# Kernel optimization log

Measured on AMD Instinct MI355X. Metric: run time of the kernel, lower is better.

## Reference

```python
import jax, jax.numpy as jnp
import numpy as np

HEADS = 8
DIM_HEAD = 64
DIM = 512
MAX_POS_EMB = 512
SCALE = DIM_HEAD ** -0.5


def setup_inputs() -> dict:
    key = jax.random.key(0)
    ks = jax.random.split(key, 6)
    B, N = 2, 2048
    inner = HEADS * DIM_HEAD  # 512
    x = jax.random.normal(ks[0], (B, N, DIM), dtype=jnp.float32)
    # torch Linear weights stored as [out, in]; we keep [in, out] for x @ W
    Wq = jax.random.normal(ks[1], (DIM, inner), dtype=jnp.float32) * (DIM ** -0.5)
    Wkv = jax.random.normal(ks[2], (DIM, 2 * inner), dtype=jnp.float32) * (DIM ** -0.5)
    Wo = jax.random.normal(ks[3], (inner, DIM), dtype=jnp.float32) * (inner ** -0.5)
    bo = jax.random.normal(ks[4], (DIM,), dtype=jnp.float32) * 0.02
    rel_emb = jax.random.normal(ks[5], (2 * MAX_POS_EMB + 1, DIM_HEAD), dtype=jnp.float32)
    return {"x": x, "Wq": Wq, "Wkv": Wkv, "Wo": Wo, "bo": bo, "rel_emb": rel_emb}


def reference(x, Wq, Wkv, Wo, bo, rel_emb):
    B, N, _ = x.shape
    h, d = HEADS, DIM_HEAD
    q = x @ Wq                                # [B, N, h*d]
    kv = x @ Wkv                              # [B, N, 2*h*d]
    k, v = jnp.split(kv, 2, axis=-1)
    to_heads = lambda t: t.reshape(B, N, h, d).transpose(0, 2, 1, 3)  # [B, h, N, d]
    q, k, v = to_heads(q), to_heads(k), to_heads(v)

    dots = jnp.einsum('bhid,bhjd->bhij', q, k) * SCALE  # [B, h, N, N]

    # relative positional bias: dist clamped to [-max, max], shifted to [0, 2*max]
    seq = jnp.arange(N)
    dist = jnp.clip(seq[:, None] - seq[None, :], -MAX_POS_EMB, MAX_POS_EMB) + MAX_POS_EMB
    rel = rel_emb[dist]                                 # [N, N, d]
    pos_attn = jnp.einsum('bhnd,njd->bhnj', q, rel) * SCALE
    dots = dots + pos_attn

    attn = jax.nn.softmax(dots, axis=-1)
    out = jnp.einsum('bhij,bhjd->bhid', attn, v)        # [B, h, N, d]
    out = out.transpose(0, 2, 1, 3).reshape(B, N, h * d)
    return out @ Wo + bo
```

## Files before the change

kernel.cpp:

```cpp
#include <hip/hip_runtime.h>
#include <hip/hip_bf16.h>
#include <stdint.h>

#define HEADS 8
#define DHEAD 64
#define DIM 512
#define NSEQ 2048
#define BATCH 2
#define NROWS (BATCH * NSEQ)
#define QKV_N 1536
#define REL_ROWS 1025
#define REL_PITCH 1088
#define NSPLIT 2
#define KV_PER_SPLIT (NSEQ / NSPLIT)

static constexpr float SCALE_LOG2E = 0.125f * 1.4426950408889634f;

typedef __attribute__((ext_vector_type(8))) short bf16x8;
typedef __attribute__((ext_vector_type(4))) float f32x4;

__device__ __forceinline__ uint16_t f2bf(float f) {
    union { float f; uint32_t u; } v{f};
    uint32_t r = (v.u + 0x7FFFu + ((v.u >> 16) & 1u)) >> 16;
    return (uint16_t)r;
}
__device__ __forceinline__ float bf2f(uint16_t u) {
    union { uint32_t u; float f; } v{(uint32_t)u << 16};
    return v.f;
}

__global__ void prep_misc(const float* __restrict__ x, const float* __restrict__ rel,
                          uint16_t* __restrict__ xb, uint16_t* __restrict__ relb) {
    int total = NROWS * DIM + REL_PITCH * DHEAD;
    for (int idx = blockIdx.x * blockDim.x + threadIdx.x; idx < total; idx += gridDim.x * blockDim.x) {
        if (idx < NROWS * DIM) {
            xb[idx] = f2bf(x[idx]);
        } else {
            int i2 = idx - NROWS * DIM;
            relb[i2] = (i2 < REL_ROWS * DHEAD) ? f2bf(rel[i2]) : (uint16_t)0;
        }
    }
}

__global__ void prep_w(const float* __restrict__ Wq, const float* __restrict__ Wkv,
                       const float* __restrict__ Wo,
                       uint16_t* __restrict__ Wqkv_t, uint16_t* __restrict__ Wo_t) {
    __shared__ float tile[32][33];
    int bid = blockIdx.x;
    const float* src; uint16_t* dst; int J, ti, tj;
    if (bid < 256)      { src = Wq;  dst = Wqkv_t;             J = 512;  ti = bid >> 4;        tj = bid & 15; }
    else if (bid < 768) { int b = bid - 256; src = Wkv; dst = Wqkv_t + 512 * 512; J = 1024; ti = b >> 5; tj = b & 31; }
    else                { int b = bid - 768; src = Wo;  dst = Wo_t;   J = 512;  ti = b >> 4;        tj = b & 15; }
    int tx = threadIdx.x & 31, ty = threadIdx.x >> 5;
    int k0 = ti * 32, j0 = tj * 32;
    #pragma unroll
    for (int i = 0; i < 4; i++) tile[ty + 8 * i][tx] = src[(size_t)(k0 + ty + 8 * i) * J + j0 + tx];
    __syncthreads();
    #pragma unroll
    for (int i = 0; i < 4; i++) dst[(size_t)(j0 + ty + 8 * i) * 512 + k0 + tx] = f2bf(tile[tx][ty + 8 * i]);
}

template <bool BF16_OUT>
__global__ __launch_bounds__(256) void gemm128(const uint16_t* __restrict__ A,
                                               const uint16_t* __restrict__ Bt,
                                               void* __restrict__ Cout,
                                               const float* __restrict__ bias,
                                               int K, int ldc) {
    __shared__ char lds[32768];
    char* ldsA = lds;
    char* ldsB = lds + 16384;
    int m0 = blockIdx.x * 128, n0 = blockIdx.y * 128;
    int t = threadIdx.x, lane = t & 63, w = t >> 6;
    int wr = w >> 1, wc = w & 1;
    int l15 = lane & 15, lh = lane >> 4;
    f32x4 acc[4][4] = {};
    for (int k0 = 0; k0 < K; k0 += 64) {
        __syncthreads();
        {
            int row = t >> 3, ch = t & 7;
            #pragma unroll
            for (int p = 0; p < 4; p++) {
                int r = row + 32 * p;
                bf16x8 va = *(const bf16x8*)(A + (size_t)(m0 + r) * K + k0 + ch * 8);
                *(bf16x8*)(ldsA + r * 128 + ((ch * 16) ^ ((r & 7) << 4))) = va;
                bf16x8 vb = *(const bf16x8*)(Bt + (size_t)(n0 + r) * K + k0 + ch * 8);
                *(bf16x8*)(ldsB + r * 128 + ((ch * 16) ^ ((r & 7) << 4))) = vb;
            }
        }
        __syncthreads();
        #pragma unroll
        for (int kk = 0; kk < 2; kk++) {
            bf16x8 a[4], b[4];
            #pragma unroll
            for (int mi = 0; mi < 4; mi++) {
                int m = wr * 64 + mi * 16 + l15;
                a[mi] = *(const bf16x8*)(ldsA + m * 128 + ((kk * 64 + lh * 16) ^ ((m & 7) << 4)));
            }
            #pragma unroll
            for (int ni = 0; ni < 4; ni++) {
                int n = wc * 64 + ni * 16 + l15;
                b[ni] = *(const bf16x8*)(ldsB + n * 128 + ((kk * 64 + lh * 16) ^ ((n & 7) << 4)));
            }
            #pragma unroll
            for (int mi = 0; mi < 4; mi++)
                #pragma unroll
                for (int ni = 0; ni < 4; ni++)
                    acc[mi][ni] = __builtin_amdgcn_mfma_f32_16x16x32_bf16(a[mi], b[ni], acc[mi][ni], 0, 0, 0);
        }
    }
    #pragma unroll
    for (int mi = 0; mi < 4; mi++)
        #pragma unroll
        for (int ni = 0; ni < 4; ni++)
            #pragma unroll
            for (int i = 0; i < 4; i++) {
                int m = m0 + wr * 64 + mi * 16 + lh * 4 + i;
                int n = n0 + wc * 64 + ni * 16 + l15;
                float v = acc[mi][ni][i];
                if constexpr (BF16_OUT) ((uint16_t*)Cout)[(size_t)m * ldc + n] = f2bf(v);
                else                    ((float*)Cout)[(size_t)m * ldc + n] = v + bias[n];
            }
}

__global__ __launch_bounds__(256) void qrel_gemm(const uint16_t* __restrict__ QKV,
                                                 const uint16_t* __restrict__ relb,
                                                 uint16_t* __restrict__ qrel) {
    __shared__ char lds[16384];
    char* ldsA = lds;
    char* ldsB = lds + 8192;
    int h = blockIdx.y;
    int r0 = blockIdx.x * 64;
    int t = threadIdx.x, lane = t & 63, w = t >> 6;
    int l15 = lane & 15, lh = lane >> 4;
    {
        int row = t >> 3, ch = t & 7;
        #pragma unroll
        for (int p = 0; p < 2; p++) {
            int r = row + 32 * p;
            bf16x8 v = *(const bf16x8*)(QKV + (size_t)(r0 + r) * QKV_N + h * 64 + ch * 8);
            *(bf16x8*)(ldsA + r * 128 + ((ch * 16) ^ ((r & 7) << 4))) = v;
        }
    }
    __syncthreads();
    bf16x8 afrag[2];
    #pragma unroll
    for (int kk = 0; kk < 2; kk++) {
        int m = w * 16 + l15;
        afrag[kk] = *(const bf16x8*)(ldsA + m * 128 + ((kk * 64 + lh * 16) ^ ((m & 7) << 4)));
    }
    for (int pb = 0; pb < REL_PITCH / 64; pb++) {
        int p0 = pb * 64;
        __syncthreads();
        {
            int row = t >> 3, ch = t & 7;
            #pragma unroll
            for (int p = 0; p < 2; p++) {
                int r = row + 32 * p;
                bf16x8 v = *(const bf16x8*)(relb + (size_t)(p0 + r) * 64 + ch * 8);
                *(bf16x8*)(ldsB + r * 128 + ((ch * 16) ^ ((r & 7) << 4))) = v;
            }
        }
        __syncthreads();
        f32x4 acc[4] = {};
        #pragma unroll
        for (int kk = 0; kk < 2; kk++)
            #pragma unroll
            for (int ni = 0; ni < 4; ni++) {
                int n = ni * 16 + l15;
                bf16x8 b = *(const bf16x8*)(ldsB + n * 128 + ((kk * 64 + lh * 16) ^ ((n & 7) << 4)));
                acc[ni] = __builtin_amdgcn_mfma_f32_16x16x32_bf16(afrag[kk], b, acc[ni], 0, 0, 0);
            }
        #pragma unroll
        for (int ni = 0; ni < 4; ni++)
            #pragma unroll
            for (int i = 0; i < 4; i++) {
                int rr = r0 + w * 16 + lh * 4 + i;
                int p = p0 + ni * 16 + l15;
                qrel[((size_t)h * NROWS + rr) * REL_PITCH + p] = f2bf(acc[ni][i]);
            }
    }
}

__global__ __launch_bounds__(512, 4) void attn_kernel(const uint16_t* __restrict__ QKV,
                                                      const uint16_t* __restrict__ qrel,
                                                      float* __restrict__ Opart,
                                                      float* __restrict__ mlpart) {
    __shared__ char lds[53248];
    char* ldsQ = lds;
    char* ldsKV = lds + 16384;

    int flat = blockIdx.x + 16 * (blockIdx.y + 8 * blockIdx.z);
    int x = (flat & 7) * 64 + (flat >> 3);
    int qb = x & 15, h = (x >> 4) & 7, z = x >> 7;
    int b = z >> 1, sp = z & 1;

    int t = threadIdx.x, lane = t & 63, w = t >> 6;
    int l15 = lane & 15, lh = lane >> 4;
    int row = t >> 3, ch = t & 7;
    int n0 = qb * 128;
    int kvbase = sp * KV_PER_SPLIT;
    size_t rowQ = (size_t)b * NSEQ + n0;

    {
        int buf = t >> 8, idx = t & 255;
        uint32_t val = (idx < 16) ? 0x3F803F80u : 0u;
        char* p = ldsKV + buf * 18432 + 8192 + 8192 + (idx >> 4) * 128 + (idx & 15) * 8;
        *(uint32_t*)(p) = val;
        *(uint32_t*)(p + 4) = val;
    }

    #pragma unroll
    for (int p = 0; p < 2; p++) {
        int r = row + 64 * p;
        bf16x8 v = *(const bf16x8*)(QKV + (rowQ + r) * QKV_N + h * 64 + ch * 8);
        *(bf16x8*)(ldsQ + r * 128 + ((ch * 16) ^ ((r & 7) << 4))) = v;
    }
    __syncthreads();
    bf16x8 qf[2];
    #pragma unroll
    for (int kk = 0; kk < 2; kk++) {
        int m = w * 16 + l15;
        qf[kk] = *(const bf16x8*)(ldsQ + m * 128 + ((kk * 64 + lh * 16) ^ ((m & 7) << 4)));
    }
    char* myP = ldsQ + w * 2048;

    f32x4 oacc[5] = {};
    float mrow[4];
    #pragma unroll
    for (int i = 0; i < 4; i++) mrow[i] = -INFINITY;

    const uint16_t* qbase = qrel + ((size_t)h * NROWS + (size_t)b * NSEQ) * REL_PITCH;
    uint32_t rowbase[4];
    #pragma unroll
    for (int i = 0; i < 4; i++) rowbase[i] = (uint32_t)(n0 + w * 16 + lh * 4 + i) * REL_PITCH + 512;

    auto load_kv = [&](int tile, bf16x8& kr, bf16x8& vr) {
        size_t gro = ((size_t)b * NSEQ + kvbase + tile * 64 + row) * QKV_N + h * 64 + ch * 8;
        kr = *(const bf16x8*)(QKV + gro + 512);
        vr = *(const bf16x8*)(QKV + gro + 1024);
    };
    auto scatter_kv = [&](int tile, bf16x8& kr, bf16x8& vr) {
        char* ldsK = ldsKV + (tile & 1) * 18432;
        char* ldsV = ldsK + 8192;
        *(bf16x8*)(ldsK + row * 128 + ((ch * 16) ^ ((row & 7) << 4))) = kr;
        #pragma unroll
        for (int dd = 0; dd < 8; dd++) {
            int d = ch * 8 + dd;
            int s = dd ^ ch;
            *(uint16_t*)(ldsV + d * 128 + 2 * (row ^ (s << 3))) = (uint16_t)vr[dd];
        }
    };
    auto load_g = [&](int tile, uint16_t* g) {
        int kv0 = kvbase + tile * 64;
        int rel0 = n0 - kv0;
        if (rel0 <= -640) {
            #pragma unroll
            for (int i = 0; i < 4; i++) {
                uint16_t v = qbase[rowbase[i] - 512];
                #pragma unroll
                for (int nf = 0; nf < 4; nf++) g[nf * 4 + i] = v;
            }
        } else if (rel0 >= 576) {
            #pragma unroll
            for (int i = 0; i < 4; i++) {
                uint16_t v = qbase[rowbase[i] + 512];
                #pragma unroll
                for (int nf = 0; nf < 4; nf++) g[nf * 4 + i] = v;
            }
        } else {
            #pragma unroll
            for (int i = 0; i < 4; i++) {
                int nmk = (n0 + w * 16 + lh * 4 + i) - kv0;
                #pragma unroll
                for (int nf = 0; nf < 4; nf++) {
                    int d = nmk - (nf * 16 + l15);
                    d = d < -512 ? -512 : (d > 512 ? 512 : d);
                    g[nf * 4 + i] = qbase[rowbase[i] + d];
                }
            }
        }
    };

    const int NT = KV_PER_SPLIT / 64;
    uint16_t gA[16], gB[16];
    bf16x8 krA, vrA, krB, vrB;

    load_kv(0, krA, vrA);
    load_g(0, gA);
    scatter_kv(0, krA, vrA);
    load_kv(1, krB, vrB);
    load_g(1, gB);

    auto body = [&](int tt, bf16x8& kS, bf16x8& vS, uint16_t* gS, bf16x8& kO, bf16x8& vO) {
        char* ldsK = ldsKV + (tt & 1) * 18432;
        char* ldsV = ldsK + 8192;
        __syncthreads();
        if (tt + 2 < NT) load_kv(tt + 2, kS, vS);

        f32x4 sacc[4] = {};
        __builtin_amdgcn_s_setprio(1);
        #pragma unroll
        for (int kk = 0; kk < 2; kk++)
            #pragma unroll
            for (int nf = 0; nf < 4; nf++) {
                int n = nf * 16 + l15;
                bf16x8 kfv = *(const bf16x8*)(ldsK + n * 128 + ((kk * 64 + lh * 16) ^ ((n & 7) << 4)));
                sacc[nf] = __builtin_amdgcn_mfma_f32_16x16x32_bf16(qf[kk], kfv, sacc[nf], 0, 0, 0);
            }
        __builtin_amdgcn_s_setprio(0);

        #pragma unroll
        for (int nf = 0; nf < 4; nf++)
            #pragma unroll
            for (int i = 0; i < 4; i++)
                sacc[nf][i] += bf2f(gS[nf * 4 + i]);
        if (tt + 2 < NT) load_g(tt + 2, gS);

        float lmax = sacc[0][0];
        #pragma unroll
        for (int nf = 0; nf < 4; nf++)
            #pragma unroll
            for (int i = 0; i < 4; i++) lmax = fmaxf(lmax, sacc[nf][i]);
        float mmin = fminf(fminf(mrow[0], mrow[1]), fminf(mrow[2], mrow[3]));
        if (!__all(lmax <= mmin + 64.0f)) {
            #pragma unroll
            for (int i = 0; i < 4; i++) {
                float mx = fmaxf(fmaxf(sacc[0][i], sacc[1][i]), fmaxf(sacc[2][i], sacc[3][i]));
                mx = fmaxf(mx, __shfl_xor(mx, 1));
                mx = fmaxf(mx, __shfl_xor(mx, 2));
                mx = fmaxf(mx, __shfl_xor(mx, 4));
                mx = fmaxf(mx, __shfl_xor(mx, 8));
                float mnew = fmaxf(mrow[i], mx);
                float alpha = exp2f((mrow[i] - mnew) * SCALE_LOG2E);
                mrow[i] = mnew;
                #pragma unroll
                for (int nf = 0; nf < 5; nf++) oacc[nf][i] *= alpha;
            }
        }

        #pragma unroll
        for (int i = 0; i < 4; i++) {
            int r = lh * 4 + i;
            int rsw = (r & 7) << 4;
            #pragma unroll
            for (int nf = 0; nf < 4; nf++) {
                float p = exp2f((sacc[nf][i] - mrow[i]) * SCALE_LOG2E);
                uint32_t pb;
                asm("v_cvt_pk_bf16_f32 %0, %1, %2" : "=v"(pb) : "v"(p), "v"(p));
                *(uint16_t*)(myP + r * 128 + (((nf * 16 + l15) * 2) ^ rsw)) = (uint16_t)pb;
            }
        }

        asm volatile("s_waitcnt lgkmcnt(0)" ::: "memory");
        __builtin_amdgcn_sched_barrier(0);
        __builtin_amdgcn_s_setprio(1);
        #pragma unroll
        for (int kk = 0; kk < 2; kk++) {
            bf16x8 pa = *(const bf16x8*)(myP + l15 * 128 + ((kk * 64 + lh * 16) ^ ((l15 & 7) << 4)));
            #pragma unroll
            for (int nf = 0; nf < 5; nf++) {
                int d = nf * 16 + l15;
                int sd = (d & 7) ^ ((d >> 3) & 7);
                bf16x8 vb = *(const bf16x8*)(ldsV + d * 128 + 16 * ((kk * 4 + lh) ^ sd));
                oacc[nf] = __builtin_amdgcn_mfma_f32_16x16x32_bf16(pa, vb, oacc[nf], 0, 0, 0);
            }
        }
        __builtin_amdgcn_s_setprio(0);

        if (tt + 1 < NT) scatter_kv(tt + 1, kO, vO);
    };

    #pragma unroll 1
    for (int tt2 = 0; tt2 < NT; tt2 += 2) {
        body(tt2,     krA, vrA, gA, krB, vrB);
        body(tt2 + 1, krB, vrB, gB, krA, vrA);
    }

    size_t rbase = ((size_t)(sp * BATCH + b) * HEADS + h) * NSEQ;
    #pragma unroll
    for (int nf = 0; nf < 4; nf++)
        #pragma unroll
        for (int i = 0; i < 4; i++) {
            int r = n0 + w * 16 + lh * 4 + i;
            Opart[(rbase + r) * 64 + nf * 16 + l15] = oacc[nf][i];
        }
    if (l15 == 0) {
        #pragma unroll
        for (int i = 0; i < 4; i++) {
            int r = n0 + w * 16 + lh * 4 + i;
            mlpart[(rbase + r) * 2]     = mrow[i];
            mlpart[(rbase + r) * 2 + 1] = oacc[4][i];
        }
    }
}

__global__ __launch_bounds__(256) void combine_kernel(const float* __restrict__ Opart,
                                                      const float* __restrict__ mlpart,
                                                      uint16_t* __restrict__ attO) {
    int lane = threadIdx.x & 63;
    int R = blockIdx.x * 4 + (threadIdx.x >> 6);
    const int SPSTRIDE = BATCH * HEADS * NSEQ;
    float m1 = mlpart[(size_t)R * 2], l1 = mlpart[(size_t)R * 2 + 1];
    float m2 = mlpart[((size_t)SPSTRIDE + R) * 2], l2 = mlpart[((size_t)SPSTRIDE + R) * 2 + 1];
    float M = fmaxf(m1, m2);
    float w1 = exp2f((m1 - M) * SCALE_LOG2E);
    float w2 = exp2f((m2 - M) * SCALE_LOG2E);
    float Linv = 1.f / (l1 * w1 + l2 * w2);
    float o1 = Opart[(size_t)R * 64 + lane];
    float o2 = Opart[((size_t)SPSTRIDE + R) * 64 + lane];
    float o = (o1 * w1 + o2 * w2) * Linv;
    int bh = R >> 11, n = R & 2047;
    int b = bh >> 3, hh = bh & 7;
    attO[((size_t)(b * NSEQ + n)) * DIM + hh * 64 + lane] = f2bf(o);
}

extern "C" void kernel_launch(void* const* d_in, const int* in_sizes, int n_in,
                              void* d_out, int out_size, void* d_ws, size_t ws_size,
                              hipStream_t stream) {
    const float* x   = (const float*)d_in[0];
    const float* Wq  = (const float*)d_in[1];
    const float* Wkv = (const float*)d_in[2];
    const float* Wo  = (const float*)d_in[3];
    const float* bo  = (const float*)d_in[4];
    const float* rel = (const float*)d_in[5];
    char* ws = (char*)d_ws;
    uint16_t* Xb     = (uint16_t*)(ws);
    float*    mlp    = (float*)(ws);
    uint16_t* Wqkv_t = (uint16_t*)(ws + 4194304);
    uint16_t* Wo_t   = (uint16_t*)(ws + 5767168);
    uint16_t* relb   = (uint16_t*)(ws + 6291456);
    uint16_t* QKV    = (uint16_t*)(ws + 6430720);
    uint16_t* attO   = (uint16_t*)(ws + 19013632);
    uint16_t* qrel   = (uint16_t*)(ws + 23207936);
    float*    Opart  = (float*)(ws + 94511104);

    prep_misc<<<2048, 256, 0, stream>>>(x, rel, Xb, relb);
    prep_w<<<1024, 256, 0, stream>>>(Wq, Wkv, Wo, Wqkv_t, Wo_t);
    gemm128<true><<<dim3(32, 12), 256, 0, stream>>>(Xb, Wqkv_t, QKV, nullptr, 512, QKV_N);
    qrel_gemm<<<dim3(64, 8), 256, 0, stream>>>(QKV, relb, qrel);
    attn_kernel<<<dim3(16, 8, 4), 512, 0, stream>>>(QKV, qrel, Opart, mlp);
    combine_kernel<<<8192, 256, 0, stream>>>(Opart, mlp, attO);
    gemm128<false><<<dim3(32, 4), 256, 0, stream>>>(attO, Wo_t, (float*)d_out, bo, 512, DIM);
}
```

Measured before the change: 159.0 us.

## Stage relative-bias window through LDS with vectorized global loads

Each thread previously gathered 16 scattered bf16 relative-bias values per KV tile straight from global memory. Now each thread loads two contiguous 8-element vectors of the diagonal window of the qrel row into registers, writes them into a new per-wave LDS region, and the MMA lanes read their bias values back from LDS with a reversed index. The aim is to replace many scalar uncoalesced global loads with a few 16-byte loads. In exchange, LDS use per block grows from 53 KB to about 70 KB, which may lower the number of resident blocks, and each tile adds LDS traffic.

Result: slower. 209.0 us (+31.4%).

```diff
diff --git a/kernel.cpp b/kernel.cpp
--- a/kernel.cpp
+++ b/kernel.cpp
@@ -17,6 +17,7 @@
 static constexpr float SCALE_LOG2E = 0.125f * 1.4426950408889634f;
 
 typedef __attribute__((ext_vector_type(8))) short bf16x8;
+typedef __attribute__((ext_vector_type(4))) short bf16x4;
 typedef __attribute__((ext_vector_type(4))) float f32x4;
 
 __device__ __forceinline__ uint16_t f2bf(float f) {
@@ -185,9 +186,10 @@
                                                       const uint16_t* __restrict__ qrel,
                                                       float* __restrict__ Opart,
                                                       float* __restrict__ mlpart) {
-    __shared__ char lds[53248];
+    __shared__ __align__(16) char lds[70656];
     char* ldsQ = lds;
     char* ldsKV = lds + 16384;
+    char* ldsW = lds + 53248;
 
     int flat = blockIdx.x + 16 * (blockIdx.y + 8 * blockIdx.z);
     int x = (flat & 7) * 64 + (flat >> 3);
@@ -197,6 +199,7 @@
     int t = threadIdx.x, lane = t & 63, w = t >> 6;
     int l15 = lane & 15, lh = lane >> 4;
     int row = t >> 3, ch = t & 7;
+    int q4 = t & 3;
     int n0 = qb * 128;
     int kvbase = sp * KV_PER_SPLIT;
     size_t rowQ = (size_t)b * NSEQ + n0;
@@ -223,6 +226,7 @@
         qf[kk] = *(const bf16x8*)(ldsQ + m * 128 + ((kk * 64 + lh * 16) ^ ((m & 7) << 4)));
     }
     char* myP = ldsQ + w * 2048;
+    char* myW = ldsW + w * 2176;
 
     f32x4 oacc[5] = {};
     float mrow[4];
@@ -230,9 +234,8 @@
     for (int i = 0; i < 4; i++) mrow[i] = -INFINITY;
 
     const uint16_t* qbase = qrel + ((size_t)h * NROWS + (size_t)b * NSEQ) * REL_PITCH;
-    uint32_t rowbase[4];
-    #pragma unroll
-    for (int i = 0; i < 4; i++) rowbase[i] = (uint32_t)(n0 + w * 16 + lh * 4 + i) * REL_PITCH + 512;
+    const uint16_t* qrow_n = qbase + (size_t)(n0 + (t >> 2)) * REL_PITCH + 512;
+    int nmk_w = n0 + (t >> 2) - kvbase;
 
     auto load_kv = [&](int tile, bf16x8& kr, bf16x8& vr) {
         size_t gro = ((size_t)b * NSEQ + kvbase + tile * 64 + row) * QKV_N + h * 64 + ch * 8;
@@ -250,52 +253,65 @@
             *(uint16_t*)(ldsV + d * 128 + 2 * (row ^ (s << 3))) = (uint16_t)vr[dd];
         }
     };
-    auto load_g = [&](int tile, uint16_t* g) {
-        int kv0 = kvbase + tile * 64;
-        int rel0 = n0 - kv0;
-        if (rel0 <= -640) {
-            #pragma unroll
-            for (int i = 0; i < 4; i++) {
-                uint16_t v = qbase[rowbase[i] - 512];
+    auto load_w = [&](int tile, bf16x8* wreg) {
+        int dbase = nmk_w - tile * 64 - 63;
+        #pragma unroll
+        for (int p = 0; p < 2; p++) {
+            int dlo = dbase + q4 * 16 + p * 8;
+            if (dlo >= -512 && dlo <= 505) {
+                wreg[p] = *(const bf16x8*)(qrow_n + dlo);
+            } else if (dlo <= -520) {
+                uint16_t v = qrow_n[-512];
                 #pragma unroll
-                for (int nf = 0; nf < 4; nf++) g[nf * 4 + i] = v;
-            }
-        } else if (rel0 >= 576) {
-            #pragma unroll
-            for (int i = 0; i < 4; i++) {
-                uint16_t v = qbase[rowbase[i] + 512];
+                for (int e = 0; e < 8; e++) wreg[p][e] = (short)v;
+            } else if (dlo >= 512) {
+                uint16_t v = qrow_n[512];
                 #pragma unroll
-                for (int nf = 0; nf < 4; nf++) g[nf * 4 + i] = v;
-            }
-        } else {
-            #pragma unroll
-            for (int i = 0; i < 4; i++) {
-                int nmk = (n0 + w * 16 + lh * 4 + i) - kv0;
+                for (int e = 0; e < 8; e++) wreg[p][e] = (short)v;
+            } else {
                 #pragma unroll
-                for (int nf = 0; nf < 4; nf++) {
-                    int d = nmk - (nf * 16 + l15);
+                for (int e = 0; e < 8; e++) {
+                    int d = dlo + e;
                     d = d < -512 ? -512 : (d > 512 ? 512 : d);
-                    g[nf * 4 + i] = qbase[rowbase[i] + d];
+                    wreg[p][e] = (short)qrow_n[d];
                 }
             }
         }
     };
+    auto write_w = [&](bf16x8* wreg) {
+        char* base = ldsW + (t >> 6) * 2176 + ((t >> 2) & 15) * 136 + q4 * 32;
+        const bf16x4* w0 = (const bf16x4*)&wreg[0];
+        const bf16x4* w1 = (const bf16x4*)&wreg[1];
+        *(bf16x4*)(base)      = w0[0];
+        *(bf16x4*)(base + 8)  = w0[1];
+        *(bf16x4*)(base + 16) = w1[0];
+        *(bf16x4*)(base + 24) = w1[1];
+    };
 
     const int NT = KV_PER_SPLIT / 64;
-    uint16_t gA[16], gB[16];
-    bf16x8 krA, vrA, krB, vrB;
+    bf16x8 krA, vrA, krB, vrB, wrA[2], wrB[2];
 
     load_kv(0, krA, vrA);
-    load_g(0, gA);
+    load_w(0, wrA);
     scatter_kv(0, krA, vrA);
+    write_w(wrA);
     load_kv(1, krB, vrB);
-    load_g(1, gB);
-
-    auto body = [&](int tt, bf16x8& kS, bf16x8& vS, uint16_t* gS, bf16x8& kO, bf16x8& vO) {
+    load_w(1, wrB);
+
+    auto body = [&](int tt, bf16x8& kS, bf16x8& vS, bf16x8* wS,
+                    bf16x8& kO, bf16x8& vO, bf16x8* wO) {
         char* ldsK = ldsKV + (tt & 1) * 18432;
         char* ldsV = ldsK + 8192;
         __syncthreads();
-        if (tt + 2 < NT) load_kv(tt + 2, kS, vS);
+        if (tt + 2 < NT) { load_kv(tt + 2, kS, vS); load_w(tt + 2, wS); }
+
+        uint16_t gb[16];
+        #pragma unroll
+        for (int nf = 0; nf < 4; nf++)
+            #pragma unroll
+            for (int i = 0; i < 4; i++)
+                gb[nf * 4 + i] = *(const uint16_t*)(myW + (lh * 4 + i) * 136
+                                                    + (63 - nf * 16 - l15) * 2);
 
         f32x4 sacc[4] = {};
         __builtin_amdgcn_s_setprio(1);
@@ -313,8 +329,7 @@
         for (int nf = 0; nf < 4; nf++)
             #pragma unroll
             for (int i = 0; i < 4; i++)
-                sacc[nf][i] += bf2f(gS[nf * 4 + i]);
-        if (tt + 2 < NT) load_g(tt + 2, gS);
+                sacc[nf][i] += bf2f(gb[nf * 4 + i]);
 
         float lmax = sacc[0][0];
         #pragma unroll
@@ -367,13 +382,13 @@
         }
         __builtin_amdgcn_s_setprio(0);
 
-        if (tt + 1 < NT) scatter_kv(tt + 1, kO, vO);
+        if (tt + 1 < NT) { scatter_kv(tt + 1, kO, vO); write_w(wO); }
     };
 
     #pragma unroll 1
     for (int tt2 = 0; tt2 < NT; tt2 += 2) {
-        body(tt2,     krA, vrA, gA, krB, vrB);
-        body(tt2 + 1, krB, vrB, gB, krA, vrA);
+        body(tt2,     krA, vrA, wrA, krB, vrB, wrB);
+        body(tt2 + 1, krB, vrB, wrB, krA, vrA, wrA);
     }
 
     size_t rbase = ((size_t)(sp * BATCH + b) * HEADS + h) * NSEQ;
```

## Fuse relative-position bias into attention kernel via on-the-fly MFMA and lane permute

Applied to the files above, without the earlier changes.

Removes the separate qrel_gemm kernel, which wrote a large per-head q·rel table (roughly 71 MB bf16) and had attention gather from it. Each attention tile now computes q·rel for the 80 relative offsets it needs using extra MFMAs on rel embedding rows loaded from global memory. A ds_bpermute then realigns the diagonal (Toeplitz) structure into the score layout. This trades a large memory write and gather for extra MFMA work, cross-lane shuffles and uncached rel loads inside the attention loop. It also simplifies the KV pipeline from a two-tile software prefetch to a single-tile one.

New measurement: 167.5 us. +5.4%, slower.

```diff
diff --git a/kernel.cpp b/kernel.cpp
--- a/kernel.cpp
+++ b/kernel.cpp
@@ -10,7 +10,7 @@
 #define NROWS (BATCH * NSEQ)
 #define QKV_N 1536
 #define REL_ROWS 1025
-#define REL_PITCH 1088
+#define REL_PITCH_ROWS 1088
 #define NSPLIT 2
 #define KV_PER_SPLIT (NSEQ / NSPLIT)
 
@@ -24,14 +24,10 @@
     uint32_t r = (v.u + 0x7FFFu + ((v.u >> 16) & 1u)) >> 16;
     return (uint16_t)r;
 }
-__device__ __forceinline__ float bf2f(uint16_t u) {
-    union { uint32_t u; float f; } v{(uint32_t)u << 16};
-    return v.f;
-}
 
 __global__ void prep_misc(const float* __restrict__ x, const float* __restrict__ rel,
                           uint16_t* __restrict__ xb, uint16_t* __restrict__ relb) {
-    int total = NROWS * DIM + REL_PITCH * DHEAD;
+    int total = NROWS * DIM + REL_PITCH_ROWS * DHEAD;
     for (int idx = blockIdx.x * blockDim.x + threadIdx.x; idx < total; idx += gridDim.x * blockDim.x) {
         if (idx < NROWS * DIM) {
             xb[idx] = f2bf(x[idx]);
@@ -122,67 +118,8 @@
             }
 }
 
-__global__ __launch_bounds__(256) void qrel_gemm(const uint16_t* __restrict__ QKV,
-                                                 const uint16_t* __restrict__ relb,
-                                                 uint16_t* __restrict__ qrel) {
-    __shared__ char lds[16384];
-    char* ldsA = lds;
-    char* ldsB = lds + 8192;
-    int h = blockIdx.y;
-    int r0 = blockIdx.x * 64;
-    int t = threadIdx.x, lane = t & 63, w = t >> 6;
-    int l15 = lane & 15, lh = lane >> 4;
-    {
-        int row = t >> 3, ch = t & 7;
-        #pragma unroll
-        for (int p = 0; p < 2; p++) {
-            int r = row + 32 * p;
-            bf16x8 v = *(const bf16x8*)(QKV + (size_t)(r0 + r) * QKV_N + h * 64 + ch * 8);
-            *(bf16x8*)(ldsA + r * 128 + ((ch * 16) ^ ((r & 7) << 4))) = v;
-        }
-    }
-    __syncthreads();
-    bf16x8 afrag[2];
-    #pragma unroll
-    for (int kk = 0; kk < 2; kk++) {
-        int m = w * 16 + l15;
-        afrag[kk] = *(const bf16x8*)(ldsA + m * 128 + ((kk * 64 + lh * 16) ^ ((m & 7) << 4)));
-    }
-    for (int pb = 0; pb < REL_PITCH / 64; pb++) {
-        int p0 = pb * 64;
-        __syncthreads();
-        {
-            int row = t >> 3, ch = t & 7;
-            #pragma unroll
-            for (int p = 0; p < 2; p++) {
-                int r = row + 32 * p;
-                bf16x8 v = *(const bf16x8*)(relb + (size_t)(p0 + r) * 64 + ch * 8);
-                *(bf16x8*)(ldsB + r * 128 + ((ch * 16) ^ ((r & 7) << 4))) = v;
-            }
-        }
-        __syncthreads();
-        f32x4 acc[4] = {};
-        #pragma unroll
-        for (int kk = 0; kk < 2; kk++)
-            #pragma unroll
-            for (int ni = 0; ni < 4; ni++) {
-                int n = ni * 16 + l15;
-                bf16x8 b = *(const bf16x8*)(ldsB + n * 128 + ((kk * 64 + lh * 16) ^ ((n & 7) << 4)));
-                acc[ni] = __builtin_amdgcn_mfma_f32_16x16x32_bf16(afrag[kk], b, acc[ni], 0, 0, 0);
-            }
-        #pragma unroll
-        for (int ni = 0; ni < 4; ni++)
-            #pragma unroll
-            for (int i = 0; i < 4; i++) {
-                int rr = r0 + w * 16 + lh * 4 + i;
-                int p = p0 + ni * 16 + l15;
-                qrel[((size_t)h * NROWS + rr) * REL_PITCH + p] = f2bf(acc[ni][i]);
-            }
-    }
-}
-
 __global__ __launch_bounds__(512, 4) void attn_kernel(const uint16_t* __restrict__ QKV,
-                                                      const uint16_t* __restrict__ qrel,
+                                                      const uint16_t* __restrict__ relb,
                                                       float* __restrict__ Opart,
                                                       float* __restrict__ mlpart) {
     __shared__ char lds[53248];
@@ -229,10 +166,10 @@
     #pragma unroll
     for (int i = 0; i < 4; i++) mrow[i] = -INFINITY;
 
-    const uint16_t* qbase = qrel + ((size_t)h * NROWS + (size_t)b * NSEQ) * REL_PITCH;
-    uint32_t rowbase[4];
-    #pragma unroll
-    for (int i = 0; i < 4; i++) rowbase[i] = (uint32_t)(n0 + w * 16 + lh * 4 + i) * REL_PITCH + 512;
+    int exAddr[4];
+    #pragma unroll
+    for (int i = 0; i < 4; i++)
+        exAddr[i] = (((lane & 48) | ((lh * 4 + i + 15 - l15) & 15)) << 2);
 
     auto load_kv = [&](int tile, bf16x8& kr, bf16x8& vr) {
         size_t gro = ((size_t)b * NSEQ + kvbase + tile * 64 + row) * QKV_N + h * 64 + ch * 8;
@@ -250,52 +187,30 @@
             *(uint16_t*)(ldsV + d * 128 + 2 * (row ^ (s << 3))) = (uint16_t)vr[dd];
         }
     };
-    auto load_g = [&](int tile, uint16_t* g) {
-        int kv0 = kvbase + tile * 64;
-        int rel0 = n0 - kv0;
-        if (rel0 <= -640) {
-            #pragma unroll
-            for (int i = 0; i < 4; i++) {
-                uint16_t v = qbase[rowbase[i] - 512];
-                #pragma unroll
-                for (int nf = 0; nf < 4; nf++) g[nf * 4 + i] = v;
-            }
-        } else if (rel0 >= 576) {
-            #pragma unroll
-            for (int i = 0; i < 4; i++) {
-                uint16_t v = qbase[rowbase[i] + 512];
-                #pragma unroll
-                for (int nf = 0; nf < 4; nf++) g[nf * 4 + i] = v;
-            }
-        } else {
-            #pragma unroll
-            for (int i = 0; i < 4; i++) {
-                int nmk = (n0 + w * 16 + lh * 4 + i) - kv0;
-                #pragma unroll
-                for (int nf = 0; nf < 4; nf++) {
-                    int d = nmk - (nf * 16 + l15);
-                    d = d < -512 ? -512 : (d > 512 ? 512 : d);
-                    g[nf * 4 + i] = qbase[rowbase[i] + d];
-                }
-            }
-        }
-    };
 
     const int NT = KV_PER_SPLIT / 64;
-    uint16_t gA[16], gB[16];
-    bf16x8 krA, vrA, krB, vrB;
-
-    load_kv(0, krA, vrA);
-    load_g(0, gA);
-    scatter_kv(0, krA, vrA);
-    load_kv(1, krB, vrB);
-    load_g(1, gB);
-
-    auto body = [&](int tt, bf16x8& kS, bf16x8& vS, uint16_t* gS, bf16x8& kO, bf16x8& vO) {
+    bf16x8 kr, vr;
+    load_kv(0, kr, vr);
+    scatter_kv(0, kr, vr);
+
+    #pragma unroll 1
+    for (int tt = 0; tt < NT; ++tt) {
         char* ldsK = ldsKV + (tt & 1) * 18432;
         char* ldsV = ldsK + 8192;
         __syncthreads();
-        if (tt + 2 < NT) load_kv(tt + 2, kS, vS);
+
+        int dlo = n0 + w * 16 - (kvbase + tt * 64) - 63;
+        bf16x8 rfr[5][2];
+        #pragma unroll
+        for (int f = 0; f < 5; f++) {
+            int d = dlo + f * 16 + l15;
+            d = d < -512 ? -512 : (d > 512 ? 512 : d);
+            const uint16_t* rp = relb + (d + 512) * 64 + lh * 8;
+            rfr[f][0] = *(const bf16x8*)(rp);
+            rfr[f][1] = *(const bf16x8*)(rp + 32);
+        }
+        bool pf = (tt + 1 < NT);
+        if (pf) load_kv(tt + 1, kr, vr);
 
         f32x4 sacc[4] = {};
         __builtin_amdgcn_s_setprio(1);
@@ -307,14 +222,25 @@
                 bf16x8 kfv = *(const bf16x8*)(ldsK + n * 128 + ((kk * 64 + lh * 16) ^ ((n & 7) << 4)));
                 sacc[nf] = __builtin_amdgcn_mfma_f32_16x16x32_bf16(qf[kk], kfv, sacc[nf], 0, 0, 0);
             }
+        f32x4 rect[5] = {};
+        #pragma unroll
+        for (int f = 0; f < 5; f++) {
+            rect[f] = __builtin_amdgcn_mfma_f32_16x16x32_bf16(qf[0], rfr[f][0], rect[f], 0, 0, 0);
+            rect[f] = __builtin_amdgcn_mfma_f32_16x16x32_bf16(qf[1], rfr[f][1], rect[f], 0, 0, 0);
+        }
         __builtin_amdgcn_s_setprio(0);
 
         #pragma unroll
-        for (int nf = 0; nf < 4; nf++)
-            #pragma unroll
-            for (int i = 0; i < 4; i++)
-                sacc[nf][i] += bf2f(gS[nf * 4 + i]);
-        if (tt + 2 < NT) load_g(tt + 2, gS);
+        for (int i = 0; i < 4; i++) {
+            bool hi = (l15 < lh * 4 + i);
+            #pragma unroll
+            for (int nf = 0; nf < 4; nf++) {
+                float v = hi ? rect[4 - nf][i] : rect[3 - nf][i];
+                union { float f; int s; } un{v};
+                un.s = __builtin_amdgcn_ds_bpermute(exAddr[i], un.s);
+                sacc[nf][i] += un.f;
+            }
+        }
 
         float lmax = sacc[0][0];
         #pragma unroll
@@ -367,13 +293,7 @@
         }
         __builtin_amdgcn_s_setprio(0);
 
-        if (tt + 1 < NT) scatter_kv(tt + 1, kO, vO);
-    };
-
-    #pragma unroll 1
-    for (int tt2 = 0; tt2 < NT; tt2 += 2) {
-        body(tt2,     krA, vrA, gA, krB, vrB);
-        body(tt2 + 1, krB, vrB, gB, krA, vrA);
+        if (pf) scatter_kv(tt + 1, kr, vr);
     }
 
     size_t rbase = ((size_t)(sp * BATCH + b) * HEADS + h) * NSEQ;
@@ -424,21 +344,19 @@
     const float* bo  = (const float*)d_in[4];
     const float* rel = (const float*)d_in[5];
     char* ws = (char*)d_ws;
-    uint16_t* Xb     = (uint16_t*)(ws);
     float*    mlp    = (float*)(ws);
-    uint16_t* Wqkv_t = (uint16_t*)(ws + 4194304);
-    uint16_t* Wo_t   = (uint16_t*)(ws + 5767168);
-    uint16_t* relb   = (uint16_t*)(ws + 6291456);
-    uint16_t* QKV    = (uint16_t*)(ws + 6430720);
-    uint16_t* attO   = (uint16_t*)(ws + 19013632);
-    uint16_t* qrel   = (uint16_t*)(ws + 23207936);
-    float*    Opart  = (float*)(ws + 94511104);
+    uint16_t* Wo_t   = (uint16_t*)(ws + 524288);
+    uint16_t* relb   = (uint16_t*)(ws + 1048576);
+    uint16_t* attO   = (uint16_t*)(ws + 1310720);
+    uint16_t* QKV    = (uint16_t*)(ws + 5505024);
+    float*    Opart  = (float*)(ws + 18087936);
+    uint16_t* Xb     = (uint16_t*)(ws + 18087936);
+    uint16_t* Wqkv_t = (uint16_t*)(ws + 22282240);
 
     prep_misc<<<2048, 256, 0, stream>>>(x, rel, Xb, relb);
     prep_w<<<1024, 256, 0, stream>>>(Wq, Wkv, Wo, Wqkv_t, Wo_t);
     gemm128<true><<<dim3(32, 12), 256, 0, stream>>>(Xb, Wqkv_t, QKV, nullptr, 512, QKV_N);
-    qrel_gemm<<<dim3(64, 8), 256, 0, stream>>>(QKV, relb, qrel);
-    attn_kernel<<<dim3(16, 8, 4), 512, 0, stream>>>(QKV, qrel, Opart, mlp);
+    attn_kernel<<<dim3(16, 8, 4), 512, 0, stream>>>(QKV, relb, Opart, mlp);
     combine_kernel<<<8192, 256, 0, stream>>>(Opart, mlp, attO);
     gemm128<false><<<dim3(32, 4), 256, 0, stream>>>(attO, Wo_t, (float*)d_out, bo, 512, DIM);
 }
```
